# Performance work log

Hardware: AMD Instinct MI355X
Metric: run time of the kernel (lower is better)

The kernel has to match this reference:

```python
import jax, jax.numpy as jnp
import numpy as np

N_NODES = 50000
N_EDGES = 400000
N_GRAPHS = 512
F = 32        # num_features
NB = 32       # mp_num_basis_fn
ZMAX = 118
CUTOFF = 5.0
NSPH = 9      # (mp_max_degree+1)^2 with max_degree=2
DEG_IDX = jnp.array([0, 1, 1, 1, 2, 2, 2, 2, 2])  # degree of each spherical component


def _bernstein(u, n=NB):
    # reciprocal_bernstein radial basis: Bernstein polynomials of degree n-1 at u in [0,1)
    k = jnp.arange(n, dtype=jnp.float32)
    log_binom = (jax.scipy.special.gammaln(float(n)) - jax.scipy.special.gammaln(k + 1.0)
                 - jax.scipy.special.gammaln(float(n) - k))
    u = jnp.clip(u, 1e-7, 1.0 - 1e-7)[..., None]
    return jnp.exp(log_binom + k * jnp.log(u) + (float(n) - 1.0 - k) * jnp.log1p(-u))


def _smooth_cutoff(r, cutoff=CUTOFF):
    t = r / cutoff
    return jnp.where(t < 1.0, jnp.exp(1.0 - 1.0 / jnp.clip(1.0 - t * t, 1e-7, None)), 0.0)


def _sph(u):
    # real spherical harmonics (cartesian normalization) up to degree 2; u: (E,3) unit vectors
    x, y, z = u[:, 0], u[:, 1], u[:, 2]
    c = jnp.sqrt(jnp.float32(3.0))
    return jnp.stack([jnp.ones_like(x), y, z, x,
                      c * x * y, c * y * z, 0.5 * (3.0 * z * z - 1.0),
                      c * z * x, 0.5 * c * (x * x - y * y)], axis=-1)


def _dense(x, W, b):
    # equivariant Dense: shared kernel over spherical components, bias only on scalar (l=0)
    y = jnp.einsum('nmf,fg->nmg', x, W)
    return y.at[:, 0, :].add(b)


def _silu_gate(x):
    # equivariant silu: scalar channel gates all degrees (scalar part -> exact silu)
    return x * jax.nn.sigmoid(x[:, 0:1, :])


def setup_inputs() -> dict:
    key = jax.random.key(0)
    ks = jax.random.split(key, 24)
    s = 1.0 / np.sqrt(F)
    sb = 1.0 / np.sqrt(NB)
    inp = {
        'positions': 2.0 * jax.random.normal(ks[0], (N_NODES, 3), jnp.float32),
        'embed': jax.random.normal(ks[1], (ZMAX, F), jnp.float32),
        'Wy0': sb * jax.random.normal(ks[2], (3, NB, F), jnp.float32),
        'Wx0': sb * jax.random.normal(ks[3], (3, NB, F), jnp.float32),
        'W1_0': s * jax.random.normal(ks[4], (F, F), jnp.float32),
        'b1_0': jnp.zeros((F,), jnp.float32),
        'W2_0': s * jax.random.normal(ks[5], (F, F), jnp.float32),
        'b2_0': jnp.zeros((F,), jnp.float32),
        'c0': jnp.full((1,), 0.5, jnp.float32),
        'Wr_last': sb * jax.random.normal(ks[6], (NB, F), jnp.float32),
        'W1_1': s * jax.random.normal(ks[7], (F, F), jnp.float32),
        'b1_1': jnp.zeros((F,), jnp.float32),
        'W2_1': s * jax.random.normal(ks[8], (F, F), jnp.float32),
        'b2_1': jnp.zeros((F,), jnp.float32),
        'c1': jnp.full((1,), 0.5, jnp.float32),
        'Wro1': s * jax.random.normal(ks[9], (F, F), jnp.float32),
        'bro1': jnp.zeros((F,), jnp.float32),
        'Wro2': s * jax.random.normal(ks[10], (F, 1), jnp.float32),
        'bro2': jnp.zeros((1,), jnp.float32),
        'atomic_bias': jax.random.normal(ks[11], (ZMAX,), jnp.float32),
        'atomic_numbers': jax.random.randint(ks[12], (N_NODES,), 0, ZMAX, jnp.int32),
        'dst_idx': jax.random.randint(ks[13], (N_EDGES,), 0, N_NODES, jnp.int32),
        'src_idx': jax.random.randint(ks[14], (N_EDGES,), 0, N_NODES, jnp.int32),
        'batch_segments': jnp.sort(jax.random.randint(ks[15], (N_NODES,), 0, N_GRAPHS, jnp.int32)),
        'graph_mask': jnp.ones((N_GRAPHS,), jnp.bool_),
    }
    return inp


def reference(positions, embed, Wy0, Wx0, W1_0, b1_0, W2_0, b2_0, c0,
              Wr_last, W1_1, b1_1, W2_1, b2_1, c1,
              Wro1, bro1, Wro2, bro2, atomic_bias,
              atomic_numbers, dst_idx, src_idx, batch_segments, graph_mask):
    # --- edge geometry (gather_src/gather_dst) ---
    disp = positions[src_idx] - positions[dst_idx]                # (E,3)
    r = jnp.sqrt(jnp.sum(disp * disp, axis=-1) + 1e-12)           # (E,)
    u = disp / r[:, None]
    Y = _sph(u)                                                   # (E,9)
    rbf = _bernstein(r / (r + 1.0)) * _smooth_cutoff(r)[:, None]  # (E,NB)

    # --- atomic embedding, lifted to (N, 9, F) with zero higher degrees ---
    x0 = embed[atomic_numbers]                                    # (N,F)
    x = jnp.concatenate([x0[:, None, :], jnp.zeros((N_NODES, NSPH - 1, F), x0.dtype)], axis=1)

    # --- iteration 0: full-degree equivariant message pass ---
    wy = jnp.einsum('eb,lbf->elf', rbf, Wy0)[:, DEG_IDX, :]       # (E,9,F) radial weights, (0,l)->l path
    wx = jnp.einsum('eb,lbf->elf', rbf, Wx0)[:, DEG_IDX, :]       # (l,0)->l path
    xs = x[src_idx]                                               # (E,9,F)
    msg = wy * Y[:, :, None] * xs[:, 0:1, :] + wx * xs
    y = jax.ops.segment_sum(msg, dst_idx, num_segments=N_NODES)   # (N,9,F)
    y = x + y
    y = _silu_gate(_dense(y, W1_0, b1_0))
    y = _dense(y, W2_0, b2_0)
    x = x + jax.nn.silu(c0) * y                                   # y_nl == 0 (era disabled)

    # --- iteration 1 (last): max_degree=0 message pass, then reduce to scalars ---
    w0 = rbf @ Wr_last                                            # (E,F)
    msg0 = w0 * x[src_idx, 0, :]
    y0 = jax.ops.segment_sum(msg0, dst_idx, num_segments=N_NODES) # (N,F)
    xs0 = x[:, 0, :]                                              # change_max_degree -> scalars
    y0 = xs0 + y0
    y0 = jax.nn.silu(y0 @ W1_1 + b1_1)
    y0 = y0 @ W2_1 + b2_1
    xs0 = xs0 + jax.nn.silu(c1) * y0

    # --- atomic readout and per-graph sum ---
    h = jax.nn.silu(xs0 @ Wro1 + bro1)
    e_atom = (h @ Wro2)[:, 0] + bro2[0] + atomic_bias[atomic_numbers]
    e_graph = jax.ops.segment_sum(e_atom, batch_segments, num_segments=N_GRAPHS)
    return jnp.where(graph_mask, e_graph, 0.0)
```

## Files before the change

### kernel.cpp

```cpp
#include <hip/hip_runtime.h>
#include <math.h>

#define NNODES 50000
#define NEDGES 400000
#define NGRAPHS 512
#define FDIM 32
#define CAP 32

static constexpr float BINOM31[32] = {
    1.f, 31.f, 465.f, 4495.f, 31465.f, 169911.f, 736281.f, 2629575.f,
    7888725.f, 20160075.f, 44352165.f, 84672315.f, 141120525.f, 206253075.f,
    265182525.f, 300540195.f, 300540195.f, 265182525.f, 206253075.f,
    141120525.f, 84672315.f, 44352165.f, 20160075.f, 7888725.f, 2629575.f,
    736281.f, 169911.f, 31465.f, 4495.f, 465.f, 31.f, 1.f
};

__device__ __forceinline__ float fast_rcp(float x) {
    return __builtin_amdgcn_rcpf(x);
}
__device__ __forceinline__ float silu(float x) {
    return x * fast_rcp(1.0f + __expf(-x));
}

__global__ __launch_bounds__(256) void prep(
    const float* __restrict__ pos,
    const float* __restrict__ Wy0, const float* __restrict__ Wx0,
    const float* __restrict__ Wr_last,
    float4* __restrict__ pos4, int* __restrict__ deg,
    float* __restrict__ out,
    float* __restrict__ cwA, float* __restrict__ cwB)
{
    int i = blockIdx.x * 256 + threadIdx.x;
    if (i < NGRAPHS) out[i] = 0.0f;
    if (i < FDIM * FDIM) {
        float b = BINOM31[i >> 5];
        cwA[i] = b * (Wy0[i] + Wx0[i]);
        cwB[i] = b * Wr_last[i];
    }
    if (i < NNODES) {
        pos4[i] = make_float4(pos[3 * i], pos[3 * i + 1], pos[3 * i + 2], 0.f);
        deg[i] = 0;
    }
}

__global__ __launch_bounds__(256) void build_csr(
    const float4* __restrict__ pos4,
    const int* __restrict__ srci, const int* __restrict__ dsti,
    const int* __restrict__ Z,
    float4* __restrict__ pay, int* __restrict__ deg)
{
    int e = blockIdx.x * 256 + threadIdx.x;
    if (e >= NEDGES) return;
    int s = srci[e], d = dsti[e];
    float4 ps = pos4[s];
    float4 pd = pos4[d];
    float dx = ps.x - pd.x, dy = ps.y - pd.y, dz = ps.z - pd.z;
    float r = sqrtf(dx * dx + dy * dy + dz * dz + 1e-12f);
    if (r >= 5.0f) return;

    float t = r * 0.2f;
    float q = fmaxf(1.0f - t * t, 1e-7f);
    float cut = __expf(1.0f - fast_rcp(q));
    float v = fast_rcp(r + 1.0f);
    float v2 = v * v, v4 = v2 * v2, v8 = v4 * v4, v16 = v8 * v8;
    float scale = v16 * v8 * v4 * v2 * v * cut;

    int rank = atomicAdd(&deg[d], 1);
    if (rank < CAP)
        pay[(size_t)d * CAP + rank] =
            make_float4(r, scale,
                        __int_as_float(s * FDIM),
                        __int_as_float(Z[s] * FDIM));
}

__global__ __launch_bounds__(256) void pad_slots(
    float4* __restrict__ pay, int* __restrict__ deg)
{
    int n = blockIdx.x * 256 + threadIdx.x;
    if (n >= NNODES) return;
    int d = min(deg[n], CAP);
    int dr = (d + 3) & ~3;
    float4 zf = make_float4(0.f, 0.f, 0.f, 0.f);
    for (int j = d; j < dr; ++j) pay[(size_t)n * CAP + j] = zf;
    deg[n] = dr;
}

#define DECLC(CW, K) float C##K = (CW)[(K) * FDIM + f];
#define DECL_ALL_C(CW)                                                      \
    DECLC(CW,0)  DECLC(CW,1)  DECLC(CW,2)  DECLC(CW,3)  DECLC(CW,4)        \
    DECLC(CW,5)  DECLC(CW,6)  DECLC(CW,7)  DECLC(CW,8)  DECLC(CW,9)        \
    DECLC(CW,10) DECLC(CW,11) DECLC(CW,12) DECLC(CW,13) DECLC(CW,14)       \
    DECLC(CW,15) DECLC(CW,16) DECLC(CW,17) DECLC(CW,18) DECLC(CW,19)       \
    DECLC(CW,20) DECLC(CW,21) DECLC(CW,22) DECLC(CW,23) DECLC(CW,24)       \
    DECLC(CW,25) DECLC(CW,26) DECLC(CW,27) DECLC(CW,28) DECLC(CW,29)       \
    DECLC(CW,30) DECLC(CW,31)

#define HEO(KE, KO)                                                        \
    _ea = fmaf(_ea, _r2a, C##KE); _oa = fmaf(_oa, _r2a, C##KO);            \
    _eb = fmaf(_eb, _r2b, C##KE); _ob = fmaf(_ob, _r2b, C##KO);            \
    _ec = fmaf(_ec, _r2c, C##KE); _oc = fmaf(_oc, _r2c, C##KO);            \
    _ed = fmaf(_ed, _r2d, C##KE); _od = fmaf(_od, _r2d, C##KO);

#define GATHER_PIPE(ACC, XSRC, ROWSEL)                                     \
    float ACC = 0.0f;                                                      \
    if (dgr > 0) {                                                         \
        float4 _pa = _h0, _pb = _h1, _pc = _h2, _pd = _h3;                 \
        for (int j = 0; ; j += 4) {                                        \
            float _xa = (XSRC)[__float_as_int(_pa.ROWSEL) + f];            \
            float _xb = (XSRC)[__float_as_int(_pb.ROWSEL) + f];            \
            float _xc = (XSRC)[__float_as_int(_pc.ROWSEL) + f];            \
            float _xd = (XSRC)[__float_as_int(_pd.ROWSEL) + f];            \
            bool _more = (j + 4) < dgr;                                    \
            float4 _na, _nb, _nc, _nd;                                     \
            if (_more) {                                                   \
                _na = slot[j + 4]; _nb = slot[j + 5];                      \
                _nc = slot[j + 6]; _nd = slot[j + 7];                      \
            }                                                              \
            float _r2a = _pa.x * _pa.x, _r2b = _pb.x * _pb.x;              \
            float _r2c = _pc.x * _pc.x, _r2d = _pd.x * _pd.x;              \
            float _ea = C30, _oa = C31, _eb = C30, _ob = C31;              \
            float _ec = C30, _oc = C31, _ed = C30, _od = C31;              \
            HEO(28, 29) HEO(26, 27) HEO(24, 25) HEO(22, 23) HEO(20, 21)   \
            HEO(18, 19) HEO(16, 17) HEO(14, 15) HEO(12, 13) HEO(10, 11)   \
            HEO(8, 9)   HEO(6, 7)   HEO(4, 5)   HEO(2, 3)   HEO(0, 1)     \
            float _wa = fmaf(_pa.x, _oa, _ea);                             \
            float _wb = fmaf(_pb.x, _ob, _eb);                             \
            float _wc = fmaf(_pc.x, _oc, _ec);                             \
            float _wd = fmaf(_pd.x, _od, _ed);                             \
            ACC = fmaf(_pa.y * _wa, _xa, ACC);                             \
            ACC = fmaf(_pb.y * _wb, _xb, ACC);                             \
            ACC = fmaf(_pc.y * _wc, _xc, ACC);                             \
            ACC = fmaf(_pd.y * _wd, _xd, ACC);                             \
            if (!_more) break;                                             \
            _pa = _na; _pb = _nb; _pc = _nc; _pd = _nd;                    \
        }                                                                  \
    }

#define MATVEC32L(RES, WL, YP, BIAS) do {                                  \
    float4 _q0=(YP)[0], _q1=(YP)[1], _q2=(YP)[2], _q3=(YP)[3];             \
    float4 _q4=(YP)[4], _q5=(YP)[5], _q6=(YP)[6], _q7=(YP)[7];             \
    float _a0=(BIAS), _a1=0.f, _a2=0.f, _a3=0.f;                           \
    _a0=fmaf(_q0.x,(WL)[ 0*FDIM+f],_a0); _a0=fmaf(_q0.y,(WL)[ 1*FDIM+f],_a0); \
    _a0=fmaf(_q0.z,(WL)[ 2*FDIM+f],_a0); _a0=fmaf(_q0.w,(WL)[ 3*FDIM+f],_a0); \
    _a1=fmaf(_q1.x,(WL)[ 4*FDIM+f],_a1); _a1=fmaf(_q1.y,(WL)[ 5*FDIM+f],_a1); \
    _a1=fmaf(_q1.z,(WL)[ 6*FDIM+f],_a1); _a1=fmaf(_q1.w,(WL)[ 7*FDIM+f],_a1); \
    _a2=fmaf(_q2.x,(WL)[ 8*FDIM+f],_a2); _a2=fmaf(_q2.y,(WL)[ 9*FDIM+f],_a2); \
    _a2=fmaf(_q2.z,(WL)[10*FDIM+f],_a2); _a2=fmaf(_q2.w,(WL)[11*FDIM+f],_a2); \
    _a3=fmaf(_q3.x,(WL)[12*FDIM+f],_a3); _a3=fmaf(_q3.y,(WL)[13*FDIM+f],_a3); \
    _a3=fmaf(_q3.z,(WL)[14*FDIM+f],_a3); _a3=fmaf(_q3.w,(WL)[15*FDIM+f],_a3); \
    _a0=fmaf(_q4.x,(WL)[16*FDIM+f],_a0); _a0=fmaf(_q4.y,(WL)[17*FDIM+f],_a0); \
    _a0=fmaf(_q4.z,(WL)[18*FDIM+f],_a0); _a0=fmaf(_q4.w,(WL)[19*FDIM+f],_a0); \
    _a1=fmaf(_q5.x,(WL)[20*FDIM+f],_a1); _a1=fmaf(_q5.y,(WL)[21*FDIM+f],_a1); \
    _a1=fmaf(_q5.z,(WL)[22*FDIM+f],_a1); _a1=fmaf(_q5.w,(WL)[23*FDIM+f],_a1); \
    _a2=fmaf(_q6.x,(WL)[24*FDIM+f],_a2); _a2=fmaf(_q6.y,(WL)[25*FDIM+f],_a2); \
    _a2=fmaf(_q6.z,(WL)[26*FDIM+f],_a2); _a2=fmaf(_q6.w,(WL)[27*FDIM+f],_a2); \
    _a3=fmaf(_q7.x,(WL)[28*FDIM+f],_a3); _a3=fmaf(_q7.y,(WL)[29*FDIM+f],_a3); \
    _a3=fmaf(_q7.z,(WL)[30*FDIM+f],_a3); _a3=fmaf(_q7.w,(WL)[31*FDIM+f],_a3); \
    RES = (_a0+_a1)+(_a2+_a3); } while (0)

__global__ __launch_bounds__(256, 4) void fused_a(
    const float4* __restrict__ pay, const int* __restrict__ deg,
    const float* __restrict__ embed, const int* __restrict__ Z,
    const float* __restrict__ cwA,
    const float* __restrict__ W1, const float* __restrict__ b1,
    const float* __restrict__ W2, const float* __restrict__ b2,
    const float* __restrict__ c0,
    float* __restrict__ x1buf)
{
    __shared__ __align__(16) float ylds[4][64];
    __shared__ float W1l[FDIM * FDIM];
    __shared__ float W2l[FDIM * FDIM];
    int tid = threadIdx.x;
    int widx = tid >> 6;
    int lane = tid & 63;
    int f    = lane & 31;
    int half = lane >> 5;

    int n = (blockIdx.x * 4 + widx) * 2 + half;
    const float4* slot = pay + (size_t)n * CAP;
    int dgr = deg[n];
    float4 _h0 = slot[0], _h1 = slot[1];
    float4 _h2 = slot[2], _h3 = slot[3];
    float x0 = embed[Z[n] * FDIM + f];
    DECL_ALL_C(cwA)

    for (int i = tid; i < FDIM * FDIM; i += 256) {
        W1l[i] = W1[i];
        W2l[i] = W2[i];
    }
    __syncthreads();

    GATHER_PIPE(accv, embed, w)

    float yv = x0 + accv;

    float* yrow = &ylds[widx][half * 32];
    const float4* yp = (const float4*)yrow;
    yrow[f] = yv;
    float t;
    MATVEC32L(t, W1l, yp, b1[f]);
    t = silu(t);
    yrow[f] = t;
    float u;
    MATVEC32L(u, W2l, yp, b2[f]);
    x1buf[(size_t)n * FDIM + f] = fmaf(silu(c0[0]), u, x0);
}

__global__ __launch_bounds__(256, 4) void fused_b(
    const float4* __restrict__ pay, const int* __restrict__ deg,
    const float* __restrict__ x1buf, const float* __restrict__ cwB,
    const float* __restrict__ W1, const float* __restrict__ b1,
    const float* __restrict__ W2, const float* __restrict__ b2,
    const float* __restrict__ c1,
    const float* __restrict__ Wro1, const float* __restrict__ bro1,
    const float* __restrict__ Wro2, const float* __restrict__ bro2,
    const float* __restrict__ abias, const int* __restrict__ Z,
    const int* __restrict__ segs,
    float* __restrict__ out)
{
    __shared__ __align__(16) float ylds[4][64];
    __shared__ float W1l[FDIM * FDIM];
    __shared__ float W2l[FDIM * FDIM];
    __shared__ float Wrl[FDIM * FDIM];
    __shared__ float eb[8];
    __shared__ int   sb[8];
    int tid = threadIdx.x;
    int widx = tid >> 6;
    int lane = tid & 63;
    int f    = lane & 31;
    int half = lane >> 5;

    int n = (blockIdx.x * 4 + widx) * 2 + half;
    const float4* slot = pay + (size_t)n * CAP;
    int dgr = deg[n];
    float4 _h0 = slot[0], _h1 = slot[1];
    float4 _h2 = slot[2], _h3 = slot[3];
    float x1 = x1buf[(size_t)n * FDIM + f];
    int   zn = Z[n];
    DECL_ALL_C(cwB)

    for (int i = tid; i < FDIM * FDIM; i += 256) {
        W1l[i] = W1[i];
        W2l[i] = W2[i];
        Wrl[i] = Wro1[i];
    }
    __syncthreads();

    GATHER_PIPE(accv, x1buf, z)

    float yv = x1 + accv;

    float* yrow = &ylds[widx][half * 32];
    const float4* yp = (const float4*)yrow;
    yrow[f] = yv;
    float t;
    MATVEC32L(t, W1l, yp, b1[f]);
    t = silu(t);
    yrow[f] = t;
    float u;
    MATVEC32L(u, W2l, yp, b2[f]);
    float xs0 = fmaf(silu(c1[0]), u, x1);
    yrow[f] = xs0;
    float h;
    MATVEC32L(h, Wrl, yp, bro1[f]);
    float p = silu(h) * Wro2[f];
    p += __shfl_xor(p, 16, 32);
    p += __shfl_xor(p, 8, 32);
    p += __shfl_xor(p, 4, 32);
    p += __shfl_xor(p, 2, 32);
    p += __shfl_xor(p, 1, 32);

    if (f == 0) {
        eb[widx * 2 + half] = p + bro2[0] + abias[zn];
        sb[widx * 2 + half] = segs[n];
    }
    __syncthreads();
    if (tid == 0) {
        float acc = eb[0];
        int cur = sb[0];
        #pragma unroll
        for (int i = 1; i < 8; ++i) {
            if (sb[i] == cur) acc += eb[i];
            else { atomicAdd(&out[cur], acc); cur = sb[i]; acc = eb[i]; }
        }
        atomicAdd(&out[cur], acc);
    }
}

extern "C" void kernel_launch(void* const* d_in, const int* in_sizes, int n_in,
                              void* d_out, int out_size, void* d_ws, size_t ws_size,
                              hipStream_t stream)
{
    const float* pos     = (const float*)d_in[0];
    const float* embed   = (const float*)d_in[1];
    const float* Wy0     = (const float*)d_in[2];
    const float* Wx0     = (const float*)d_in[3];
    const float* W1_0    = (const float*)d_in[4];
    const float* b1_0    = (const float*)d_in[5];
    const float* W2_0    = (const float*)d_in[6];
    const float* b2_0    = (const float*)d_in[7];
    const float* c0      = (const float*)d_in[8];
    const float* Wr_last = (const float*)d_in[9];
    const float* W1_1    = (const float*)d_in[10];
    const float* b1_1    = (const float*)d_in[11];
    const float* W2_1    = (const float*)d_in[12];
    const float* b2_1    = (const float*)d_in[13];
    const float* c1      = (const float*)d_in[14];
    const float* Wro1    = (const float*)d_in[15];
    const float* bro1    = (const float*)d_in[16];
    const float* Wro2    = (const float*)d_in[17];
    const float* bro2    = (const float*)d_in[18];
    const float* abias   = (const float*)d_in[19];
    const int*   Z       = (const int*)d_in[20];
    const int*   dsti    = (const int*)d_in[21];
    const int*   srci    = (const int*)d_in[22];
    const int*   segs    = (const int*)d_in[23];

    float* out = (float*)d_out;

    char* w = (char*)d_ws;
    float4* pay   = (float4*)w;  w += (size_t)NNODES * CAP * 16;
    float*  x1buf = (float*)w;   w += (size_t)NNODES * FDIM * 4;
    float4* pos4  = (float4*)w;  w += (size_t)NNODES * 16;
    int*    deg   = (int*)w;     w += (size_t)NNODES * 4;
    float*  cwA   = (float*)w;   w += FDIM * FDIM * 4;
    float*  cwB   = (float*)w;   w += FDIM * FDIM * 4;

    const int edgeBlocks = (NEDGES + 255) / 256;
    const int nodeBlocks = NNODES / 8;
    const int prepBlocks = (NNODES + 255) / 256;

    prep<<<prepBlocks, 256, 0, stream>>>(pos, Wy0, Wx0, Wr_last,
                                         pos4, deg, out, cwA, cwB);
    build_csr<<<edgeBlocks, 256, 0, stream>>>(pos4, srci, dsti, Z, pay, deg);
    pad_slots<<<prepBlocks, 256, 0, stream>>>(pay, deg);
    fused_a<<<nodeBlocks, 256, 0, stream>>>(pay, deg, embed, Z, cwA,
                                            W1_0, b1_0, W2_0, b2_0, c0, x1buf);
    fused_b<<<nodeBlocks, 256, 0, stream>>>(pay, deg, x1buf, cwB,
                                            W1_1, b1_1, W2_1, b2_1, c1,
                                            Wro1, bro1, Wro2, bro2,
                                            abias, Z, segs, out);
}
```

Measured before the change: 187.4 us.

## Narrow gather pipeline to two edges, drop LDS weight staging, raise occupancy

```diff
diff --git a/kernel.cpp b/kernel.cpp
--- a/kernel.cpp
+++ b/kernel.cpp
@@ -79,7 +79,7 @@
     int n = blockIdx.x * 256 + threadIdx.x;
     if (n >= NNODES) return;
     int d = min(deg[n], CAP);
-    int dr = (d + 3) & ~3;
+    int dr = (d + 1) & ~1;
     float4 zf = make_float4(0.f, 0.f, 0.f, 0.f);
     for (int j = d; j < dr; ++j) pay[(size_t)n * CAP + j] = zf;
     deg[n] = dr;
@@ -97,42 +97,28 @@
 
 #define HEO(KE, KO)                                                        \
     _ea = fmaf(_ea, _r2a, C##KE); _oa = fmaf(_oa, _r2a, C##KO);            \
-    _eb = fmaf(_eb, _r2b, C##KE); _ob = fmaf(_ob, _r2b, C##KO);            \
-    _ec = fmaf(_ec, _r2c, C##KE); _oc = fmaf(_oc, _r2c, C##KO);            \
-    _ed = fmaf(_ed, _r2d, C##KE); _od = fmaf(_od, _r2d, C##KO);
+    _eb = fmaf(_eb, _r2b, C##KE); _ob = fmaf(_ob, _r2b, C##KO);
 
 #define GATHER_PIPE(ACC, XSRC, ROWSEL)                                     \
     float ACC = 0.0f;                                                      \
     if (dgr > 0) {                                                         \
-        float4 _pa = _h0, _pb = _h1, _pc = _h2, _pd = _h3;                 \
-        for (int j = 0; ; j += 4) {                                        \
+        float4 _pa = _h0, _pb = _h1;                                       \
+        for (int j = 0; ; j += 2) {                                        \
             float _xa = (XSRC)[__float_as_int(_pa.ROWSEL) + f];            \
             float _xb = (XSRC)[__float_as_int(_pb.ROWSEL) + f];            \
-            float _xc = (XSRC)[__float_as_int(_pc.ROWSEL) + f];            \
-            float _xd = (XSRC)[__float_as_int(_pd.ROWSEL) + f];            \
-            bool _more = (j + 4) < dgr;                                    \
-            float4 _na, _nb, _nc, _nd;                                     \
-            if (_more) {                                                   \
-                _na = slot[j + 4]; _nb = slot[j + 5];                      \
-                _nc = slot[j + 6]; _nd = slot[j + 7];                      \
-            }                                                              \
+            float4 _na = slot[j + 2];                                      \
+            float4 _nb = slot[j + 3];                                      \
             float _r2a = _pa.x * _pa.x, _r2b = _pb.x * _pb.x;              \
-            float _r2c = _pc.x * _pc.x, _r2d = _pd.x * _pd.x;              \
             float _ea = C30, _oa = C31, _eb = C30, _ob = C31;              \
-            float _ec = C30, _oc = C31, _ed = C30, _od = C31;              \
             HEO(28, 29) HEO(26, 27) HEO(24, 25) HEO(22, 23) HEO(20, 21)   \
             HEO(18, 19) HEO(16, 17) HEO(14, 15) HEO(12, 13) HEO(10, 11)   \
             HEO(8, 9)   HEO(6, 7)   HEO(4, 5)   HEO(2, 3)   HEO(0, 1)     \
             float _wa = fmaf(_pa.x, _oa, _ea);                             \
             float _wb = fmaf(_pb.x, _ob, _eb);                             \
-            float _wc = fmaf(_pc.x, _oc, _ec);                             \
-            float _wd = fmaf(_pd.x, _od, _ed);                             \
             ACC = fmaf(_pa.y * _wa, _xa, ACC);                             \
             ACC = fmaf(_pb.y * _wb, _xb, ACC);                             \
-            ACC = fmaf(_pc.y * _wc, _xc, ACC);                             \
-            ACC = fmaf(_pd.y * _wd, _xd, ACC);                             \
-            if (!_more) break;                                             \
-            _pa = _na; _pb = _nb; _pc = _nc; _pd = _nd;                    \
+            if (j + 2 >= dgr) break;                                       \
+            _pa = _na; _pb = _nb;                                          \
         }                                                                  \
     }
 
@@ -158,7 +144,7 @@
     _a3=fmaf(_q7.z,(WL)[30*FDIM+f],_a3); _a3=fmaf(_q7.w,(WL)[31*FDIM+f],_a3); \
     RES = (_a0+_a1)+(_a2+_a3); } while (0)
 
-__global__ __launch_bounds__(256, 4) void fused_a(
+__global__ __launch_bounds__(256, 7) void fused_a(
     const float4* __restrict__ pay, const int* __restrict__ deg,
     const float* __restrict__ embed, const int* __restrict__ Z,
     const float* __restrict__ cwA,
@@ -168,8 +154,6 @@
     float* __restrict__ x1buf)
 {
     __shared__ __align__(16) float ylds[4][64];
-    __shared__ float W1l[FDIM * FDIM];
-    __shared__ float W2l[FDIM * FDIM];
     int tid = threadIdx.x;
     int widx = tid >> 6;
     int lane = tid & 63;
@@ -180,15 +164,8 @@
     const float4* slot = pay + (size_t)n * CAP;
     int dgr = deg[n];
     float4 _h0 = slot[0], _h1 = slot[1];
-    float4 _h2 = slot[2], _h3 = slot[3];
     float x0 = embed[Z[n] * FDIM + f];
     DECL_ALL_C(cwA)
-
-    for (int i = tid; i < FDIM * FDIM; i += 256) {
-        W1l[i] = W1[i];
-        W2l[i] = W2[i];
-    }
-    __syncthreads();
 
     GATHER_PIPE(accv, embed, w)
 
@@ -198,15 +175,15 @@
     const float4* yp = (const float4*)yrow;
     yrow[f] = yv;
     float t;
-    MATVEC32L(t, W1l, yp, b1[f]);
+    MATVEC32L(t, W1, yp, b1[f]);
     t = silu(t);
     yrow[f] = t;
     float u;
-    MATVEC32L(u, W2l, yp, b2[f]);
+    MATVEC32L(u, W2, yp, b2[f]);
     x1buf[(size_t)n * FDIM + f] = fmaf(silu(c0[0]), u, x0);
 }
 
-__global__ __launch_bounds__(256, 4) void fused_b(
+__global__ __launch_bounds__(256, 7) void fused_b(
     const float4* __restrict__ pay, const int* __restrict__ deg,
     const float* __restrict__ x1buf, const float* __restrict__ cwB,
     const float* __restrict__ W1, const float* __restrict__ b1,
@@ -219,9 +196,6 @@
     float* __restrict__ out)
 {
     __shared__ __align__(16) float ylds[4][64];
-    __shared__ float W1l[FDIM * FDIM];
-    __shared__ float W2l[FDIM * FDIM];
-    __shared__ float Wrl[FDIM * FDIM];
     __shared__ float eb[8];
     __shared__ int   sb[8];
     int tid = threadIdx.x;
@@ -234,17 +208,9 @@
     const float4* slot = pay + (size_t)n * CAP;
     int dgr = deg[n];
     float4 _h0 = slot[0], _h1 = slot[1];
-    float4 _h2 = slot[2], _h3 = slot[3];
     float x1 = x1buf[(size_t)n * FDIM + f];
     int   zn = Z[n];
     DECL_ALL_C(cwB)
-
-    for (int i = tid; i < FDIM * FDIM; i += 256) {
-        W1l[i] = W1[i];
-        W2l[i] = W2[i];
-        Wrl[i] = Wro1[i];
-    }
-    __syncthreads();
 
     GATHER_PIPE(accv, x1buf, z)
 
@@ -254,15 +220,15 @@
     const float4* yp = (const float4*)yrow;
     yrow[f] = yv;
     float t;
-    MATVEC32L(t, W1l, yp, b1[f]);
+    MATVEC32L(t, W1, yp, b1[f]);
     t = silu(t);
     yrow[f] = t;
     float u;
-    MATVEC32L(u, W2l, yp, b2[f]);
+    MATVEC32L(u, W2, yp, b2[f]);
     float xs0 = fmaf(silu(c1[0]), u, x1);
     yrow[f] = xs0;
     float h;
-    MATVEC32L(h, Wrl, yp, bro1[f]);
+    MATVEC32L(h, Wro1, yp, bro1[f]);
     float p = silu(h) * Wro2[f];
     p += __shfl_xor(p, 16, 32);
     p += __shfl_xor(p, 8, 32);
```

After: 194.8 us. +3.9%, slower.
